# Performance work log

Measured on AMD Instinct MI355X. Metric: run time of the kernel, lower is better.

## Reference

```python
import jax, jax.numpy as jnp
import numpy as np

C = 512
HEADS = 4
GROUPS = 32
EPS = 1e-6


def setup_inputs() -> dict:
    key = jax.random.key(0)
    ks = jax.random.split(key, 6)
    s = 1.0 / np.sqrt(C)
    return {
        "x": jax.random.normal(ks[0], (2, C, 64, 64), dtype=jnp.float32),
        "gn_scale": jnp.ones((C,), jnp.float32),
        "gn_bias": jnp.zeros((C,), jnp.float32),
        "wq": jax.random.normal(ks[1], (C, C), jnp.float32) * s,
        "bq": jnp.zeros((C,), jnp.float32),
        "wk": jax.random.normal(ks[2], (C, C), jnp.float32) * s,
        "bk": jnp.zeros((C,), jnp.float32),
        "wv": jax.random.normal(ks[3], (C, C), jnp.float32) * s,
        "bv": jnp.zeros((C,), jnp.float32),
        "wo": jax.random.normal(ks[4], (C, C), jnp.float32) * s,
        "bo": jnp.zeros((C,), jnp.float32),
    }


def group_norm(x, scale, bias):
    # x: [b, c, h, w]; GroupNorm with 32 groups, eps 1e-6, affine
    b, c, h, w = x.shape
    xg = x.reshape(b, GROUPS, c // GROUPS, h, w)
    mean = jnp.mean(xg, axis=(2, 3, 4), keepdims=True)
    var = jnp.var(xg, axis=(2, 3, 4), keepdims=True)
    xg = (xg - mean) * jax.lax.rsqrt(var + EPS)
    x = xg.reshape(b, c, h, w)
    return x * scale[None, :, None, None] + bias[None, :, None, None]


def conv1x1(x, w, b):
    # 1x1 conv == per-pixel linear: [b,c,h,w] x [o,c] -> [b,o,h,w]
    return jnp.einsum('bchw,oc->bohw', x, w) + b[None, :, None, None]


def reference(x, gn_scale, gn_bias, wq, bq, wk, bk, wv, bv, wo, bo):
    b, c, h, w = x.shape
    hc = c // HEADS
    n = h * w

    h_ = group_norm(x, gn_scale, gn_bias)
    q = conv1x1(h_, wq, bq).reshape(b, HEADS, hc, n)
    k = conv1x1(h_, wk, bk).reshape(b, HEADS, hc, n)
    v = conv1x1(h_, wv, bv).reshape(b, HEADS, hc, n)

    # NOTE: scale uses full channel count c (repo quirk), not head_channel
    scale = jnp.asarray(c, x.dtype) ** -0.5
    scores = jnp.einsum('bhcn,bhcm->bhnm', q, k) * scale  # [b,H,N,N]
    attn = jax.nn.softmax(scores, axis=-1)
    out = jnp.einsum('bhnm,bhcm->bhcn', attn, v)  # [b,H,hc,N]

    out = out.reshape(b, c, h, w)
    return x + conv1x1(out, wo, bo)
```

## Files before the change

kernel.cpp:

```cpp
#include <hip/hip_runtime.h>

typedef float    f32x4 __attribute__((ext_vector_type(4)));
typedef short    bf16x8 __attribute__((ext_vector_type(8)));
typedef unsigned short u16;
typedef u16      u16x4 __attribute__((ext_vector_type(4)));
typedef unsigned u32;
typedef u32      u32x4 __attribute__((ext_vector_type(4)));

#define MFMA16(a, b, c) __builtin_amdgcn_mfma_f32_16x16x32_bf16((a), (b), (c), 0, 0, 0)

#define CCH 512
#define NPIX 4096
#define NHEAD 4
#define HC 128
#define NSPLIT 2
#define KVCHUNK (NPIX / NSPLIT)
#define QK_SCALE 0.04419417382415922f
#define LOG2E 1.4426950408889634f

__device__ __forceinline__ u16 f2b(float f) {
  unsigned u = __builtin_bit_cast(unsigned, f);
  u += 0x7FFFu + ((u >> 16) & 1u);
  return (u16)(u >> 16);
}
__device__ __forceinline__ float b2f(u16 b) {
  return __builtin_bit_cast(float, ((unsigned)b) << 16);
}

__device__ __forceinline__ void gl_lds16(const u16* g, u16* l) {
  __builtin_amdgcn_global_load_lds((const __attribute__((address_space(1))) void*)g,
                                   (__attribute__((address_space(3))) void*)l, 16, 0, 0);
}

__global__ void wconv_k(const float* __restrict__ w0, const float* __restrict__ w1,
                        const float* __restrict__ w2, const float* __restrict__ w3,
                        u16* __restrict__ dst) {
  int m = blockIdx.y;
  const float* src = (m == 0) ? w0 : (m == 1) ? w1 : (m == 2) ? w2 : w3;
  int i = (blockIdx.x * 256 + threadIdx.x) * 4;
  f32x4 v = *(const f32x4*)(src + i);
  u16x4 o = { f2b(v[0]), f2b(v[1]), f2b(v[2]), f2b(v[3]) };
  *(u16x4*)(dst + (size_t)m * (CCH * CCH) + i) = o;
}

__global__ void gn_stats_k(const float* __restrict__ x, float* __restrict__ stats) {
  int bg = blockIdx.x;
  const f32x4* p = (const f32x4*)(x + (size_t)bg * 65536);
  int t = threadIdx.x, wv = t >> 6, l = t & 63;
  float s = 0.f, ss = 0.f;
  for (int i = t; i < 16384; i += 256) {
    f32x4 v = p[i];
    s  += v[0] + v[1] + v[2] + v[3];
    ss += v[0]*v[0] + v[1]*v[1] + v[2]*v[2] + v[3]*v[3];
  }
  #pragma unroll
  for (int d = 32; d; d >>= 1) { s += __shfl_down(s, d, 64); ss += __shfl_down(ss, d, 64); }
  __shared__ float red[8];
  if (l == 0) { red[wv*2] = s; red[wv*2+1] = ss; }
  __syncthreads();
  if (t == 0) {
    s  = red[0] + red[2] + red[4] + red[6];
    ss = red[1] + red[3] + red[5] + red[7];
    float mean = s * (1.f/65536.f);
    float var  = ss * (1.f/65536.f) - mean*mean;
    stats[bg*2]   = mean;
    stats[bg*2+1] = rsqrtf(var + 1e-6f);
  }
}

__global__ void gn_norm_k(const float* __restrict__ x, const float* __restrict__ gns,
                          const float* __restrict__ gnb, const float* __restrict__ stats,
                          u16* __restrict__ Ht) {
  int t = threadIdx.x;
  int ct = blockIdx.x * 64, nt = blockIdx.y * 64, b = blockIdx.z;
  int c0 = ct + (t & 15) * 4;
  int n0 = nt + (t >> 4) * 4;
  const float* xb = x + ((size_t)b * CCH + c0) * NPIX + n0;
  int sidx = (b * 32 + (c0 >> 4)) * 2;
  float mean = stats[sidx], rstd = stats[sidx + 1];
  f32x4 rows[4];
  #pragma unroll
  for (int j = 0; j < 4; ++j) {
    f32x4 v = *(const f32x4*)(xb + (size_t)j * NPIX);
    float a  = rstd * gns[c0 + j];
    float bb = gnb[c0 + j] - mean * a;
    rows[j] = v * a + bb;
  }
  #pragma unroll
  for (int i = 0; i < 4; ++i) {
    u16x4 o = { f2b(rows[0][i]), f2b(rows[1][i]), f2b(rows[2][i]), f2b(rows[3][i]) };
    *(u16x4*)(Ht + ((size_t)b * NPIX + n0 + i) * CCH + c0) = o;
  }
}

template<int MODE>
__global__ __launch_bounds__(256) void gemm_nt(const u16* __restrict__ A,
                                               const u16* __restrict__ B,
                                               const float* __restrict__ bias,
                                               u16* __restrict__ outb,
                                               float* __restrict__ outf,
                                               const float* __restrict__ resid,
                                               float alpha) {
  __shared__ __align__(16) u16 As[128 * 32];
  __shared__ __align__(16) u16 Bs[128 * 32];
  const int t = threadIdx.x, l = t & 63, wv = t >> 6;
  const int l16 = l & 15, lq = l >> 4;
  const int mt = blockIdx.x * 128, nt = blockIdx.y * 128, z = blockIdx.z;
  const u16* Ap = A + (size_t)mt * CCH;
  const u16* Bp = (MODE == 0) ? (B + (size_t)nt * CCH)
                              : (B + ((size_t)z * NPIX + nt) * CCH);
  const int wm = (wv >> 1) * 64, wn = (wv & 1) * 64;
  f32x4 acc[4][4] = {};
  for (int k0 = 0; k0 < CCH; k0 += 32) {
    __syncthreads();
    #pragma unroll
    for (int j = 0; j < 2; ++j) {
      int idx = t + j * 256;
      int row = idx >> 2, kc = (idx & 3) * 8;
      gl_lds16(Ap + (size_t)row * CCH + k0 + kc, As + idx * 8);
      gl_lds16(Bp + (size_t)row * CCH + k0 + kc, Bs + idx * 8);
    }
    __syncthreads();
    bf16x8 af[4], bfr[4];
    #pragma unroll
    for (int i = 0; i < 4; ++i) {
      af[i]  = *(const bf16x8*)(As + (wm + i * 16 + l16) * 32 + lq * 8);
      bfr[i] = *(const bf16x8*)(Bs + (wn + i * 16 + l16) * 32 + lq * 8);
    }
    #pragma unroll
    for (int mi = 0; mi < 4; ++mi)
      #pragma unroll
      for (int ni = 0; ni < 4; ++ni)
        acc[mi][ni] = MFMA16(af[mi], bfr[ni], acc[mi][ni]);
  }
  #pragma unroll
  for (int mi = 0; mi < 4; ++mi)
    #pragma unroll
    for (int ni = 0; ni < 4; ++ni)
      #pragma unroll
      for (int r = 0; r < 4; ++r) {
        int grow = mt + wm + mi * 16 + lq * 4 + r;
        int gcol = nt + wn + ni * 16 + l16;
        float v = acc[mi][ni][r];
        if (MODE == 0) {
          outb[(size_t)grow * CCH + gcol] = f2b((v + bias[gcol]) * alpha);
        } else if (MODE == 1) {
          outb[((size_t)z * CCH + grow) * NPIX + gcol] = f2b(v + bias[grow]);
        } else {
          size_t off = ((size_t)z * CCH + grow) * NPIX + gcol;
          outf[off] = v + bias[grow] + resid[off];
        }
      }
}

__global__ __launch_bounds__(256, 2) void flash_k(const u16* __restrict__ Qt,
                                                  const u16* __restrict__ Kt,
                                                  const u16* __restrict__ Vc,
                                                  u16* __restrict__ sl0, u16* __restrict__ sl1,
                                                  float* __restrict__ mlp) {
  __shared__ __align__(16) char lds[65536];
  const int t = threadIdx.x, wv = t >> 6, l = t & 63;
  const int l16 = l & 15, lq = l >> 4;
  const int orig = blockIdx.x;
  const int gid = (orig & 7) * 64 + (orig >> 3);
  const int qx = gid & 31, grp = gid >> 5;
  const int hd = grp & 3, b = (grp >> 2) & 1, s = grp >> 3;
  const int qt0 = qx * 128 + wv * 32;

  const u16* Q = Qt + ((size_t)b * NPIX + qt0) * CCH + hd * HC;
  const u16* Kbase = Kt + (size_t)b * NPIX * CCH + hd * HC;
  const u16* Vbase = Vc + (size_t)b * CCH * NPIX + (size_t)hd * HC * NPIX;
  u16* slab = (s == 0) ? sl0 : sl1;
  u16* Ob = slab + ((size_t)(b * NHEAD + hd) * NPIX + qt0) * HC;
  size_t mlR0 = (size_t)s * 32768 + (size_t)(b * NHEAD + hd) * NPIX + qt0;

  bf16x8 qf[2][4];
  #pragma unroll
  for (int mi = 0; mi < 2; ++mi)
    #pragma unroll
    for (int kk = 0; kk < 4; ++kk)
      qf[mi][kk] = *(const bf16x8*)(Q + (size_t)(mi * 16 + l16) * CCH + kk * 32 + lq * 8);

  const int m_beg = s * KVCHUNK;
  const int sw = (l16 & 7) << 4;
  const int vb2 = (lq & 1) * 32 + (lq >> 1) * 16;

  int kbase[4], vbase[2];
  #pragma unroll
  for (int kk = 0; kk < 4; ++kk) kbase[kk] = l16 * 256 + ((kk * 64 + lq * 16) ^ sw);
  #pragma unroll
  for (int ks = 0; ks < 2; ++ks) vbase[ks] = 32768 + l16 * 128 + ((ks * 64 + vb2) ^ sw);

  u32 kgo[4], vgo[4];
  #pragma unroll
  for (int j = 0; j < 4; ++j) {
    int g = j * 256 + t;
    { int row = g >> 4, src = ((g & 15) << 4) ^ ((row & 7) << 4);
      kgo[j] = (u32)row * CCH + (src >> 1); }
    { int row = g >> 3, src = ((g & 7) << 4) ^ ((row & 7) << 4);
      vgo[j] = (u32)row * NPIX + (src >> 1); }
  }

  const short one_bf = (short)0x3F80;
  const bf16x8 vones = { one_bf, one_bf, one_bf, one_bf, one_bf, one_bf, one_bf, one_bf };

  f32x4 oacc[2][8] = {};
  f32x4 osum[2] = {};

  {
    const u16* kg = Kbase + (size_t)m_beg * CCH;
    const u16* vg = Vbase + m_beg;
    #pragma unroll
    for (int j = 0; j < 4; ++j) {
      gl_lds16(kg + kgo[j], (u16*)lds + (j * 256 + t) * 8);
      gl_lds16(vg + vgo[j], (u16*)(lds + 32768) + (j * 256 + t) * 8);
    }
  }
  asm volatile("s_waitcnt vmcnt(0)" ::: "memory");
  __syncthreads();

  const int NT = KVCHUNK / 64;

#define FLASH_BODY(CUR, M0, DOSTAGE)                                                   \
  {                                                                                    \
    if (DOSTAGE) {                                                                     \
      const u16* kg = Kbase + (size_t)((M0) + 64) * CCH;                               \
      const u16* vg = Vbase + ((M0) + 64);                                             \
      _Pragma("unroll")                                                                \
      for (int j = 0; j < 4; ++j) {                                                    \
        gl_lds16(kg + kgo[j], (u16*)(lds + ((CUR) ^ 1) * 16384) + (j * 256 + t) * 8);  \
        gl_lds16(vg + vgo[j], (u16*)(lds + 32768 + ((CUR) ^ 1) * 16384) + (j * 256 + t) * 8); \
      }                                                                                \
    }                                                                                  \
    f32x4 S[2][4] = {};                                                                \
    __builtin_amdgcn_s_setprio(1);                                                     \
    _Pragma("unroll")                                                                  \
    for (int kk = 0; kk < 4; ++kk)                                                     \
      _Pragma("unroll")                                                                \
      for (int mm = 0; mm < 4; ++mm) {                                                 \
        bf16x8 kf = *(const bf16x8*)(lds + kbase[kk] + mm * 4096 + (CUR) * 16384);     \
        S[0][mm] = MFMA16(kf, qf[0][kk], S[0][mm]);                                    \
        S[1][mm] = MFMA16(kf, qf[1][kk], S[1][mm]);                                    \
      }                                                                                \
    __builtin_amdgcn_s_setprio(0);                                                     \
    u32 pk[2][4][2];                                                                   \
    _Pragma("unroll")                                                                  \
    for (int mi = 0; mi < 2; ++mi) {                                                   \
      _Pragma("unroll")                                                                \
      for (int mm = 0; mm < 4; ++mm) {                                                 \
        f32x4 p;                                                                       \
        _Pragma("unroll")                                                              \
        for (int r = 0; r < 4; ++r) p[r] = exp2f(S[mi][mm][r]);                        \
        asm("v_cvt_pk_bf16_f32 %0, %1, %2" : "=v"(pk[mi][mm][0]) : "v"(p[0]), "v"(p[1])); \
        asm("v_cvt_pk_bf16_f32 %0, %1, %2" : "=v"(pk[mi][mm][1]) : "v"(p[2]), "v"(p[3])); \
      }                                                                                \
    }                                                                                  \
    bf16x8 pa[2][2];                                                                   \
    _Pragma("unroll")                                                                  \
    for (int mi = 0; mi < 2; ++mi)                                                     \
      _Pragma("unroll")                                                                \
      for (int ks = 0; ks < 2; ++ks) {                                                 \
        u32 a0 = pk[mi][2 * ks][0], a1 = pk[mi][2 * ks][1];                            \
        u32 b0 = pk[mi][2 * ks + 1][0], b1 = pk[mi][2 * ks + 1][1];                    \
        asm("v_permlane16_swap_b32 %0, %1" : "+v"(a0), "+v"(b0));                      \
        asm("v_permlane16_swap_b32 %0, %1" : "+v"(a1), "+v"(b1));                      \
        u32x4 w = { a0, a1, b0, b1 };                                                  \
        pa[mi][ks] = __builtin_bit_cast(bf16x8, w);                                    \
      }                                                                                \
    __builtin_amdgcn_s_setprio(1);                                                     \
    _Pragma("unroll")                                                                  \
    for (int ks = 0; ks < 2; ++ks) {                                                   \
      osum[0] = MFMA16(pa[0][ks], vones, osum[0]);                                     \
      osum[1] = MFMA16(pa[1][ks], vones, osum[1]);                                     \
      _Pragma("unroll")                                                                \
      for (int cc = 0; cc < 8; ++cc) {                                                 \
        bf16x8 vf = *(const bf16x8*)(lds + vbase[ks] + cc * 2048 + (CUR) * 16384);     \
        oacc[0][cc] = MFMA16(pa[0][ks], vf, oacc[0][cc]);                              \
        oacc[1][cc] = MFMA16(pa[1][ks], vf, oacc[1][cc]);                              \
      }                                                                                \
    }                                                                                  \
    __builtin_amdgcn_s_setprio(0);                                                     \
    asm volatile("s_waitcnt vmcnt(0)" ::: "memory");                                   \
    __syncthreads();                                                                   \
  }

  for (int it = 0; it < NT; it += 2) {
    FLASH_BODY(0, m_beg + it * 64, true)
    FLASH_BODY(1, m_beg + it * 64 + 64, (it + 2 < NT))
  }
#undef FLASH_BODY

  #pragma unroll
  for (int mi = 0; mi < 2; ++mi)
    #pragma unroll
    for (int cc = 0; cc < 8; ++cc)
      #pragma unroll
      for (int r = 0; r < 4; ++r)
        Ob[(size_t)(mi * 16 + lq * 4 + r) * HC + cc * 16 + l16] = f2b(oacc[mi][cc][r]);
  if (l16 == 0) {
    #pragma unroll
    for (int mi = 0; mi < 2; ++mi)
      #pragma unroll
      for (int r = 0; r < 4; ++r)
        mlp[mlR0 + mi * 16 + lq * 4 + r] = osum[mi][r];
  }
}

__global__ void merge_k(const u16* __restrict__ s0, const u16* __restrict__ s1,
                        const float* __restrict__ ml, u16* __restrict__ Ot) {
  int t = threadIdx.x;
  int R = blockIdx.x * 32 + (t >> 3);
  int ch = (t & 7) * 16;
  float l0 = ml[R], l1 = ml[32768 + R];
  float inv = 1.f / (l0 + l1);
  float acc[16] = {};
  const u16* sp[2] = { s0, s1 };
  #pragma unroll
  for (int s = 0; s < 2; ++s) {
    const bf16x8* p = (const bf16x8*)(sp[s] + (size_t)R * HC + ch);
    #pragma unroll
    for (int j = 0; j < 2; ++j) {
      bf16x8 v = p[j];
      #pragma unroll
      for (int e = 0; e < 8; ++e) acc[j * 8 + e] += b2f((u16)v[e]);
    }
  }
  int b = R >> 14, h = (R >> 12) & 3, q = R & 4095;
  u16* o = Ot + ((size_t)((b << 12) + q) * CCH) + h * HC + ch;
  #pragma unroll
  for (int j = 0; j < 4; ++j) {
    u16x4 o4 = { f2b(acc[j*4] * inv), f2b(acc[j*4+1] * inv),
                 f2b(acc[j*4+2] * inv), f2b(acc[j*4+3] * inv) };
    *(u16x4*)(o + j * 4) = o4;
  }
}

extern "C" void kernel_launch(void* const* d_in, const int* in_sizes, int n_in,
                              void* d_out, int out_size, void* d_ws, size_t ws_size,
                              hipStream_t stream) {
  const float* x   = (const float*)d_in[0];
  const float* gns = (const float*)d_in[1];
  const float* gnb = (const float*)d_in[2];
  const float* wq  = (const float*)d_in[3];
  const float* bq  = (const float*)d_in[4];
  const float* wk  = (const float*)d_in[5];
  const float* bk  = (const float*)d_in[6];
  const float* wv  = (const float*)d_in[7];
  const float* bv  = (const float*)d_in[8];
  const float* wo  = (const float*)d_in[9];
  const float* bo  = (const float*)d_in[10];
  float* out = (float*)d_out;
  char* ws = (char*)d_ws;

  u16*   wb    = (u16*)ws;
  u16*   Ht    = (u16*)(ws + (size_t)( 2u << 20));
  u16*   Qt    = (u16*)(ws + (size_t)(10u << 20));
  u16*   Kt    = (u16*)(ws + (size_t)(18u << 20));
  u16*   Vc    = (u16*)(ws + (size_t)(26u << 20));
  u16*   Ot    = (u16*)(ws + (size_t)(34u << 20));
  float* mlb   = (float*)(ws + (size_t)(42u << 20));
  float* stats = (float*)(ws + (size_t)(43u << 20));
  u16*   sl0   = Ht;
  u16*   sl1   = (u16*)d_out;

  wconv_k   <<<dim3(256, 4, 1), 256, 0, stream>>>(wq, wk, wv, wo, wb);
  gn_stats_k<<<dim3(64, 1, 1),  256, 0, stream>>>(x, stats);
  gn_norm_k <<<dim3(8, 64, 2),  256, 0, stream>>>(x, gns, gnb, stats, Ht);
  gemm_nt<0><<<dim3(64, 4, 1),  256, 0, stream>>>(Ht, wb + 0u * 262144u, bq, Qt, nullptr, nullptr, QK_SCALE * LOG2E);
  gemm_nt<0><<<dim3(64, 4, 1),  256, 0, stream>>>(Ht, wb + 1u * 262144u, bk, Kt, nullptr, nullptr, 1.0f);
  gemm_nt<1><<<dim3(4, 32, 2),  256, 0, stream>>>(wb + 2u * 262144u, Ht, bv, Vc, nullptr, nullptr, 1.0f);
  flash_k   <<<dim3(512, 1, 1), 256, 0, stream>>>(Qt, Kt, Vc, sl0, sl1, mlb);
  merge_k   <<<dim3(1024, 1, 1),256, 0, stream>>>(sl0, sl1, mlb, Ot);
  gemm_nt<2><<<dim3(4, 32, 2),  256, 0, stream>>>(wb + 3u * 262144u, Ot, bo, nullptr, out, x, 1.0f);
}
```

Baseline: 170.5 us.

## Split KV four ways, fuse Q/K projections, widen flash blocks, parallelize GN stats

Flash attention now splits the KV range four ways instead of two, uses 512-thread blocks covering 256 queries each, and merges four partial slabs. The Q and K projections run as one GEMM launch over the concatenated weights, with the epilogue routing columns to Qt or Kt. Group-norm statistics are computed as four partial sums per group in more blocks and reduced inside the normalize kernel. The aim is to raise parallelism and cut launch count, at the cost of extra slab memory traffic in the merge and more scattered partial-sum reads.

Result: faster. 162.6 us (-4.7%).

```diff
diff --git a/kernel.cpp b/kernel.cpp
--- a/kernel.cpp
+++ b/kernel.cpp
@@ -13,7 +13,7 @@
 #define NPIX 4096
 #define NHEAD 4
 #define HC 128
-#define NSPLIT 2
+#define NSPLIT 4
 #define KVCHUNK (NPIX / NSPLIT)
 #define QK_SCALE 0.04419417382415922f
 #define LOG2E 1.4426950408889634f
@@ -43,12 +43,12 @@
   *(u16x4*)(dst + (size_t)m * (CCH * CCH) + i) = o;
 }
 
-__global__ void gn_stats_k(const float* __restrict__ x, float* __restrict__ stats) {
-  int bg = blockIdx.x;
-  const f32x4* p = (const f32x4*)(x + (size_t)bg * 65536);
+__global__ void gn_stats_k(const float* __restrict__ x, float* __restrict__ pstats) {
+  int blk = blockIdx.x;
+  const f32x4* p = (const f32x4*)(x + (size_t)blk * 16384);
   int t = threadIdx.x, wv = t >> 6, l = t & 63;
   float s = 0.f, ss = 0.f;
-  for (int i = t; i < 16384; i += 256) {
+  for (int i = t; i < 4096; i += 256) {
     f32x4 v = p[i];
     s  += v[0] + v[1] + v[2] + v[3];
     ss += v[0]*v[0] + v[1]*v[1] + v[2]*v[2] + v[3]*v[3];
@@ -59,25 +59,27 @@
   if (l == 0) { red[wv*2] = s; red[wv*2+1] = ss; }
   __syncthreads();
   if (t == 0) {
-    s  = red[0] + red[2] + red[4] + red[6];
-    ss = red[1] + red[3] + red[5] + red[7];
-    float mean = s * (1.f/65536.f);
-    float var  = ss * (1.f/65536.f) - mean*mean;
-    stats[bg*2]   = mean;
-    stats[bg*2+1] = rsqrtf(var + 1e-6f);
+    pstats[blk*2]   = red[0] + red[2] + red[4] + red[6];
+    pstats[blk*2+1] = red[1] + red[3] + red[5] + red[7];
   }
 }
 
 __global__ void gn_norm_k(const float* __restrict__ x, const float* __restrict__ gns,
-                          const float* __restrict__ gnb, const float* __restrict__ stats,
+                          const float* __restrict__ gnb, const float* __restrict__ pstats,
                           u16* __restrict__ Ht) {
   int t = threadIdx.x;
   int ct = blockIdx.x * 64, nt = blockIdx.y * 64, b = blockIdx.z;
   int c0 = ct + (t & 15) * 4;
   int n0 = nt + (t >> 4) * 4;
   const float* xb = x + ((size_t)b * CCH + c0) * NPIX + n0;
-  int sidx = (b * 32 + (c0 >> 4)) * 2;
-  float mean = stats[sidx], rstd = stats[sidx + 1];
+  int g = b * 32 + (c0 >> 4);
+  const f32x4* ps = (const f32x4*)(pstats + g * 8);
+  f32x4 p0 = ps[0], p1 = ps[1];
+  float s  = p0[0] + p0[2] + p1[0] + p1[2];
+  float ss = p0[1] + p0[3] + p1[1] + p1[3];
+  float mean = s * (1.f/65536.f);
+  float var  = ss * (1.f/65536.f) - mean*mean;
+  float rstd = rsqrtf(var + 1e-6f);
   f32x4 rows[4];
   #pragma unroll
   for (int j = 0; j < 4; ++j) {
@@ -97,7 +99,9 @@
 __global__ __launch_bounds__(256) void gemm_nt(const u16* __restrict__ A,
                                                const u16* __restrict__ B,
                                                const float* __restrict__ bias,
+                                               const float* __restrict__ bias2,
                                                u16* __restrict__ outb,
+                                               u16* __restrict__ outb2,
                                                float* __restrict__ outf,
                                                const float* __restrict__ resid,
                                                float alpha) {
@@ -107,7 +111,7 @@
   const int l16 = l & 15, lq = l >> 4;
   const int mt = blockIdx.x * 128, nt = blockIdx.y * 128, z = blockIdx.z;
   const u16* Ap = A + (size_t)mt * CCH;
-  const u16* Bp = (MODE == 0) ? (B + (size_t)nt * CCH)
+  const u16* Bp = (MODE == 3) ? (B + (size_t)nt * CCH)
                               : (B + ((size_t)z * NPIX + nt) * CCH);
   const int wm = (wv >> 1) * 64, wn = (wv & 1) * 64;
   f32x4 acc[4][4] = {};
@@ -142,35 +146,39 @@
         int grow = mt + wm + mi * 16 + lq * 4 + r;
         int gcol = nt + wn + ni * 16 + l16;
         float v = acc[mi][ni][r];
-        if (MODE == 0) {
-          outb[(size_t)grow * CCH + gcol] = f2b((v + bias[gcol]) * alpha);
-        } else if (MODE == 1) {
+        if (MODE == 1) {
           outb[((size_t)z * CCH + grow) * NPIX + gcol] = f2b(v + bias[grow]);
-        } else {
+        } else if (MODE == 2) {
           size_t off = ((size_t)z * CCH + grow) * NPIX + gcol;
           outf[off] = v + bias[grow] + resid[off];
+        } else {
+          if (gcol < 512)
+            outb[(size_t)grow * CCH + gcol] = f2b((v + bias[gcol]) * alpha);
+          else
+            outb2[(size_t)grow * CCH + (gcol - 512)] = f2b(v + bias2[gcol - 512]);
         }
       }
 }
 
-__global__ __launch_bounds__(256, 2) void flash_k(const u16* __restrict__ Qt,
+__global__ __launch_bounds__(512, 2) void flash_k(const u16* __restrict__ Qt,
                                                   const u16* __restrict__ Kt,
                                                   const u16* __restrict__ Vc,
                                                   u16* __restrict__ sl0, u16* __restrict__ sl1,
+                                                  u16* __restrict__ sl2, u16* __restrict__ sl3,
                                                   float* __restrict__ mlp) {
   __shared__ __align__(16) char lds[65536];
   const int t = threadIdx.x, wv = t >> 6, l = t & 63;
   const int l16 = l & 15, lq = l >> 4;
   const int orig = blockIdx.x;
   const int gid = (orig & 7) * 64 + (orig >> 3);
-  const int qx = gid & 31, grp = gid >> 5;
+  const int qx = gid & 15, grp = gid >> 4;
   const int hd = grp & 3, b = (grp >> 2) & 1, s = grp >> 3;
-  const int qt0 = qx * 128 + wv * 32;
+  const int qt0 = qx * 256 + wv * 32;
 
   const u16* Q = Qt + ((size_t)b * NPIX + qt0) * CCH + hd * HC;
   const u16* Kbase = Kt + (size_t)b * NPIX * CCH + hd * HC;
   const u16* Vbase = Vc + (size_t)b * CCH * NPIX + (size_t)hd * HC * NPIX;
-  u16* slab = (s == 0) ? sl0 : sl1;
+  u16* slab = (s == 0) ? sl0 : (s == 1) ? sl1 : (s == 2) ? sl2 : sl3;
   u16* Ob = slab + ((size_t)(b * NHEAD + hd) * NPIX + qt0) * HC;
   size_t mlR0 = (size_t)s * 32768 + (size_t)(b * NHEAD + hd) * NPIX + qt0;
 
@@ -191,10 +199,10 @@
   #pragma unroll
   for (int ks = 0; ks < 2; ++ks) vbase[ks] = 32768 + l16 * 128 + ((ks * 64 + vb2) ^ sw);
 
-  u32 kgo[4], vgo[4];
-  #pragma unroll
-  for (int j = 0; j < 4; ++j) {
-    int g = j * 256 + t;
+  u32 kgo[2], vgo[2];
+  #pragma unroll
+  for (int j = 0; j < 2; ++j) {
+    int g = j * 512 + t;
     { int row = g >> 4, src = ((g & 15) << 4) ^ ((row & 7) << 4);
       kgo[j] = (u32)row * CCH + (src >> 1); }
     { int row = g >> 3, src = ((g & 7) << 4) ^ ((row & 7) << 4);
@@ -211,9 +219,9 @@
     const u16* kg = Kbase + (size_t)m_beg * CCH;
     const u16* vg = Vbase + m_beg;
     #pragma unroll
-    for (int j = 0; j < 4; ++j) {
-      gl_lds16(kg + kgo[j], (u16*)lds + (j * 256 + t) * 8);
-      gl_lds16(vg + vgo[j], (u16*)(lds + 32768) + (j * 256 + t) * 8);
+    for (int j = 0; j < 2; ++j) {
+      gl_lds16(kg + kgo[j], (u16*)lds + (j * 512 + t) * 8);
+      gl_lds16(vg + vgo[j], (u16*)(lds + 32768) + (j * 512 + t) * 8);
     }
   }
   asm volatile("s_waitcnt vmcnt(0)" ::: "memory");
@@ -227,9 +235,9 @@
       const u16* kg = Kbase + (size_t)((M0) + 64) * CCH;                               \
       const u16* vg = Vbase + ((M0) + 64);                                             \
       _Pragma("unroll")                                                                \
-      for (int j = 0; j < 4; ++j) {                                                    \
-        gl_lds16(kg + kgo[j], (u16*)(lds + ((CUR) ^ 1) * 16384) + (j * 256 + t) * 8);  \
-        gl_lds16(vg + vgo[j], (u16*)(lds + 32768 + ((CUR) ^ 1) * 16384) + (j * 256 + t) * 8); \
+      for (int j = 0; j < 2; ++j) {                                                    \
+        gl_lds16(kg + kgo[j], (u16*)(lds + ((CUR) ^ 1) * 16384) + (j * 512 + t) * 8);  \
+        gl_lds16(vg + vgo[j], (u16*)(lds + 32768 + ((CUR) ^ 1) * 16384) + (j * 512 + t) * 8); \
       }                                                                                \
     }                                                                                  \
     f32x4 S[2][4] = {};                                                                \
@@ -307,16 +315,17 @@
 }
 
 __global__ void merge_k(const u16* __restrict__ s0, const u16* __restrict__ s1,
+                        const u16* __restrict__ s2, const u16* __restrict__ s3,
                         const float* __restrict__ ml, u16* __restrict__ Ot) {
   int t = threadIdx.x;
   int R = blockIdx.x * 32 + (t >> 3);
   int ch = (t & 7) * 16;
-  float l0 = ml[R], l1 = ml[32768 + R];
-  float inv = 1.f / (l0 + l1);
+  float L = ml[R] + ml[32768 + R] + ml[65536 + R] + ml[98304 + R];
+  float inv = 1.f / L;
   float acc[16] = {};
-  const u16* sp[2] = { s0, s1 };
-  #pragma unroll
-  for (int s = 0; s < 2; ++s) {
+  const u16* sp[4] = { s0, s1, s2, s3 };
+  #pragma unroll
+  for (int s = 0; s < 4; ++s) {
     const bf16x8* p = (const bf16x8*)(sp[s] + (size_t)R * HC + ch);
     #pragma unroll
     for (int j = 0; j < 2; ++j) {
@@ -360,16 +369,20 @@
   u16*   Ot    = (u16*)(ws + (size_t)(34u << 20));
   float* mlb   = (float*)(ws + (size_t)(42u << 20));
   float* stats = (float*)(ws + (size_t)(43u << 20));
+  u16*   sl3   = (u16*)(ws + (size_t)(44u << 20));
   u16*   sl0   = Ht;
   u16*   sl1   = (u16*)d_out;
+  u16*   sl2   = (u16*)((char*)d_out + (size_t)(8u << 20));
 
   wconv_k   <<<dim3(256, 4, 1), 256, 0, stream>>>(wq, wk, wv, wo, wb);
-  gn_stats_k<<<dim3(64, 1, 1),  256, 0, stream>>>(x, stats);
+  gn_stats_k<<<dim3(256, 1, 1), 256, 0, stream>>>(x, stats);
   gn_norm_k <<<dim3(8, 64, 2),  256, 0, stream>>>(x, gns, gnb, stats, Ht);
-  gemm_nt<0><<<dim3(64, 4, 1),  256, 0, stream>>>(Ht, wb + 0u * 262144u, bq, Qt, nullptr, nullptr, QK_SCALE * LOG2E);
-  gemm_nt<0><<<dim3(64, 4, 1),  256, 0, stream>>>(Ht, wb + 1u * 262144u, bk, Kt, nullptr, nullptr, 1.0f);
-  gemm_nt<1><<<dim3(4, 32, 2),  256, 0, stream>>>(wb + 2u * 262144u, Ht, bv, Vc, nullptr, nullptr, 1.0f);
-  flash_k   <<<dim3(512, 1, 1), 256, 0, stream>>>(Qt, Kt, Vc, sl0, sl1, mlb);
-  merge_k   <<<dim3(1024, 1, 1),256, 0, stream>>>(sl0, sl1, mlb, Ot);
-  gemm_nt<2><<<dim3(4, 32, 2),  256, 0, stream>>>(wb + 3u * 262144u, Ot, bo, nullptr, out, x, 1.0f);
-}
+  gemm_nt<3><<<dim3(64, 8, 1),  256, 0, stream>>>(Ht, wb, bq, bk, Qt, Kt, nullptr, nullptr,
+                                                  QK_SCALE * LOG2E);
+  gemm_nt<1><<<dim3(4, 32, 2),  256, 0, stream>>>(wb + 2u * 262144u, Ht, bv, nullptr, Vc, nullptr,
+                                                  nullptr, nullptr, 1.0f);
+  flash_k   <<<dim3(512, 1, 1), 512, 0, stream>>>(Qt, Kt, Vc, sl0, sl1, sl2, sl3, mlb);
+  merge_k   <<<dim3(1024, 1, 1),256, 0, stream>>>(sl0, sl1, sl2, sl3, mlb, Ot);
+  gemm_nt<2><<<dim3(4, 32, 2),  256, 0, stream>>>(wb + 3u * 262144u, Ot, bo, nullptr, nullptr,
+                                                  nullptr, out, x, 1.0f);
+}
```
